# Kernel optimization log

Hardware: AMD Instinct MI355X
Metric: run time of the kernel (lower is better)

## Reference

```python
import jax, jax.numpy as jnp
import numpy as np


def setup_inputs() -> dict:
    key = jax.random.key(0)
    kq, kk, kv = jax.random.split(key, 3)
    B, S, D = 4, 4096, 128
    return {
        "q_proj": jax.random.normal(kq, (B, S, D), dtype=jnp.float32),
        "k_proj": jax.random.normal(kk, (B, S, D), dtype=jnp.float32),
        "v_proj": jax.random.normal(kv, (B, S, D), dtype=jnp.float32),
    }


def reference(q_proj, k_proj, v_proj):
    # Block-wise online softmax in the original is mathematically exact
    # full (non-causal) scaled dot-product attention.
    d = q_proj.shape[-1]
    scale = 1.0 / jnp.sqrt(jnp.asarray(d, dtype=q_proj.dtype))
    logits = jnp.einsum('bqd,bkd->bqk', q_proj, k_proj) * scale  # [B,S,S]
    attn = jax.nn.softmax(logits, axis=-1)
    return jnp.einsum('bqk,bkd->bqd', attn, v_proj)
```

## Files before the change

kernel.cpp:

```cpp
#include <hip/hip_runtime.h>
#include <hip/hip_bf16.h>
#include <stdint.h>

#define Bn 4
#define Sn 4096
#define Dn 128
#define SCALE ((float)(0.08838834764831843 * 1.4426950408889634))

typedef __attribute__((ext_vector_type(8)))  short short8;
typedef __attribute__((ext_vector_type(4)))  short short4v;
typedef __attribute__((ext_vector_type(4)))  float f32x4;
typedef __attribute__((ext_vector_type(16))) float f32x16;
typedef __attribute__((ext_vector_type(2)))  uint32_t uint2v;

__device__ __forceinline__ uint32_t bfround(float f){
  union { float f; uint32_t u; } a; a.f = f;
  return a.u + 0x7FFFu + ((a.u >> 16) & 1u);
}
__device__ __forceinline__ uint32_t f2bf2(float lo, float hi){
  return (bfround(hi) & 0xFFFF0000u) | (bfround(lo) >> 16);
}
__device__ __forceinline__ uint32_t f2bf2_fast(float lo, float hi){
  const uint32_t a = __float_as_uint(lo) + 0x8000u;
  const uint32_t b = __float_as_uint(hi) + 0x8000u;
  return __builtin_amdgcn_perm(b, a, 0x07060302u);
}
__device__ __forceinline__ float bf2f(short s){
  union { uint32_t u; float f; } a; a.u = ((uint32_t)(unsigned short)s) << 16; return a.f;
}
__device__ __forceinline__ float fexp2(float x){
#if __has_builtin(__builtin_amdgcn_exp2f)
  return __builtin_amdgcn_exp2f(x);
#else
  return exp2f(x);
#endif
}

__device__ __forceinline__ void gload16(const void* g, void* l){
  __builtin_amdgcn_global_load_lds(
      (const __attribute__((address_space(1))) unsigned int*)g,
      (__attribute__((address_space(3))) unsigned int*)l, 16, 0, 0);
}

__global__ void prep_kernel(const float* __restrict__ k, const float* __restrict__ v,
                            short* __restrict__ kb, short* __restrict__ vf){
  const int bid = blockIdx.x;
  const int t   = threadIdx.x;
  if (bid < 512){
    const int b = bid >> 7, i = bid & 127;
#pragma unroll
    for (int it=0; it<2; ++it){
      const int lin = it*256 + t;
      const int ln = lin & 31;
      const int tg = lin >> 5;
      const int tt = tg >> 1, hh = tg & 1;
      const float* src = k + ((size_t)(b*Sn + i*32 + ln))*Dn + tg*8;
      const f32x4 a = *(const f32x4*)src;
      const f32x4 c = *(const f32x4*)(src + 4);
      union { uint32_t u[4]; short8 s; } pk;
      pk.u[0] = f2bf2(a[0], a[1]);
      pk.u[1] = f2bf2(a[2], a[3]);
      pk.u[2] = f2bf2(c[0], c[1]);
      pk.u[3] = f2bf2(c[2], c[3]);
      *(short8*)(kb + (((size_t)(b*128 + i)*8 + tt)*64 + (hh*32 + ln))*8) = pk.s;
    }
  } else {
    __shared__ float tile[32][132];
    const int vb = bid - 512;
    const int b = vb >> 7, i = vb & 127;
#pragma unroll
    for (int it=0; it<4; ++it){
      const int lin = it*256 + t;
      const int row = lin >> 5;
      const int c4  = lin & 31;
      const f32x4 val = *(const f32x4*)(v + ((size_t)(b*Sn + i*32 + row))*Dn + c4*4);
      tile[row][c4*4+0] = val[0];
      tile[row][c4*4+1] = val[1];
      tile[row][c4*4+2] = val[2];
      tile[row][c4*4+3] = val[3];
    }
    __syncthreads();
#pragma unroll
    for (int cc=0; cc<2; ++cc){
      const int c = cc*256 + t;
      const int l = c & 63, fidx = c >> 6;
      const int t_ = fidx >> 2, mt = fidx & 3;
      const int ln = l & 31, h5 = l >> 5;
      const int d = mt*32 + ln;
      const int kb0 = 16*t_ + 4*h5;
      union { uint32_t u[4]; short8 s; } pk;
#pragma unroll
      for (int p=0;p<4;++p){
        const int j0 = 2*p, j1 = 2*p+1;
        const int kl0 = kb0 + (j0&3) + 8*(j0>>2);
        const int kl1 = kb0 + (j1&3) + 8*(j1>>2);
        pk.u[p] = f2bf2(tile[kl0][d], tile[kl1][d]);
      }
      *(short8*)(vf + (((size_t)(b*128 + i)*8 + fidx)*64 + l)*8) = pk.s;
    }
  }
}

__global__ __launch_bounds__(128, 2) void fa_kernel(
    const float* __restrict__ Qg, const short* __restrict__ Kb,
    const short* __restrict__ VFb, short* __restrict__ parts,
    float* __restrict__ lparts){
  __shared__ __align__(16) char lds[32768];
  const int tid = threadIdx.x;
  const int w = tid >> 6, lane = tid & 63;
  const int ln = lane & 31, h5 = lane >> 5;
  const int idx = blockIdx.x;
  const int b   = idx & 3;
  const int u2  = idx >> 2;
  const int qt  = u2 & 31;
  const int ks  = u2 >> 5;
  const int q0  = qt * 128;
  const int start_it = ks*21 + (ks < 2 ? ks : 2);
  const int n_it     = 21 + (ks < 2 ? 1 : 0);

  short8 Qf[2][8];
#pragma unroll
  for (int tile=0;tile<2;++tile){
    const float* qp = Qg + ((size_t)(b*Sn + q0 + w*64 + tile*32 + ln))*Dn;
#pragma unroll
    for (int t=0;t<8;++t){
      const int d0 = t*16 + h5*8;
      const f32x4 a = *(const f32x4*)(qp + d0);
      const f32x4 c = *(const f32x4*)(qp + d0 + 4);
      union { uint32_t u[4]; short8 s; } pk;
      pk.u[0] = f2bf2(a[0]*SCALE, a[1]*SCALE);
      pk.u[1] = f2bf2(a[2]*SCALE, a[3]*SCALE);
      pk.u[2] = f2bf2(c[0]*SCALE, c[1]*SCALE);
      pk.u[3] = f2bf2(c[2]*SCALE, c[3]*SCALE);
      Qf[tile][t] = pk.s;
    }
  }

  f32x16 Ot[2][4];
#pragma unroll
  for (int tile=0;tile<2;++tile)
#pragma unroll
    for (int m=0;m<4;++m)
#pragma unroll
      for (int r=0;r<16;++r) Ot[tile][m][r] = 0.0f;
  float ls00=0.f, ls01=0.f, ls10=0.f, ls11=0.f;

  const char* gsrc0 = (w ? (const char*)VFb : (const char*)Kb)
                    + (size_t)(b*128)*8192 + (size_t)lane*16;
  auto stage = [&](int it, int ph){
    char* dst = lds + ph*16384 + (w ? 8192 : 0);
    const char* src = gsrc0 + (size_t)it*8192;
#pragma unroll
    for (int u=0;u<8;++u) gload16(src + u*1024, dst + u*1024);
  };

  stage(start_it, 0);

  for (int i=0; i<n_it; ++i){
    const int ph = i & 1;
    __syncthreads();
    if (i+1 < n_it) stage(start_it+i+1, ph^1);

    const char* bK = lds + ph*16384 + (size_t)lane*16;
    const char* bV = bK + 8192;

    f32x16 St0, St1;
#pragma unroll
    for (int r=0;r<16;++r){ St0[r] = 0.0f; St1[r] = 0.0f; }
    __builtin_amdgcn_s_setprio(1);
#pragma unroll
    for (int t=0;t<8;++t){
      const short8 kf = *(const short8*)(bK + t*1024);
      St0 = __builtin_amdgcn_mfma_f32_32x32x16_bf16(kf, Qf[0][t], St0, 0, 0, 0);
      St1 = __builtin_amdgcn_mfma_f32_32x32x16_bf16(kf, Qf[1][t], St1, 0, 0, 0);
    }
    __builtin_amdgcn_s_setprio(0);

#pragma unroll
    for (int r=0;r<16;++r) St0[r] = fexp2(St0[r]);
#pragma unroll
    for (int r=0;r<16;++r) St1[r] = fexp2(St1[r]);
#pragma unroll
    for (int r=0;r<16;r+=2){
      ls00 += St0[r]; ls01 += St0[r+1];
      ls10 += St1[r]; ls11 += St1[r+1];
    }

    union { uint32_t u[4]; short8 s; } pfA[2], pfB[2];
#pragma unroll
    for (int t=0;t<2;++t){
      pfA[t].u[0] = f2bf2_fast(St0[8*t+0], St0[8*t+1]);
      pfA[t].u[1] = f2bf2_fast(St0[8*t+2], St0[8*t+3]);
      pfA[t].u[2] = f2bf2_fast(St0[8*t+4], St0[8*t+5]);
      pfA[t].u[3] = f2bf2_fast(St0[8*t+6], St0[8*t+7]);
      pfB[t].u[0] = f2bf2_fast(St1[8*t+0], St1[8*t+1]);
      pfB[t].u[1] = f2bf2_fast(St1[8*t+2], St1[8*t+3]);
      pfB[t].u[2] = f2bf2_fast(St1[8*t+4], St1[8*t+5]);
      pfB[t].u[3] = f2bf2_fast(St1[8*t+6], St1[8*t+7]);
    }

    __builtin_amdgcn_s_setprio(1);
#pragma unroll
    for (int t=0;t<2;++t){
#pragma unroll
      for (int mt=0;mt<4;++mt){
        const short8 vf = *(const short8*)(bV + (t*4+mt)*1024);
        Ot[0][mt] = __builtin_amdgcn_mfma_f32_32x32x16_bf16(vf, pfA[t].s, Ot[0][mt], 0, 0, 0);
        Ot[1][mt] = __builtin_amdgcn_mfma_f32_32x32x16_bf16(vf, pfB[t].s, Ot[1][mt], 0, 0, 0);
      }
    }
    __builtin_amdgcn_s_setprio(0);
  }

  float lsum0 = ls00 + ls01; lsum0 += __shfl_xor(lsum0, 32, 64);
  float lsum1 = ls10 + ls11; lsum1 += __shfl_xor(lsum1, 32, 64);

  const int pslot = (b*32 + qt)*6 + ks;
#pragma unroll
  for (int tile=0;tile<2;++tile){
    short* pbase = parts + (size_t)pslot*16384 + (size_t)(w*64 + tile*32 + ln)*128;
#pragma unroll
    for (int mt=0;mt<4;++mt){
#pragma unroll
      for (int g=0;g<4;++g){
        union { uint32_t u[2]; short4v s; } o;
        o.u[0] = f2bf2(Ot[tile][mt][4*g],   Ot[tile][mt][4*g+1]);
        o.u[1] = f2bf2(Ot[tile][mt][4*g+2], Ot[tile][mt][4*g+3]);
        *(short4v*)(pbase + mt*32 + 8*g + 4*h5) = o.s;
      }
    }
  }
  if (h5 == 0){
    lparts[(size_t)pslot*128 + w*64 + ln]      = lsum0;
    lparts[(size_t)pslot*128 + w*64 + 32 + ln] = lsum1;
  }
}

__global__ void reduce_kernel(const short* __restrict__ parts,
                              const float* __restrict__ lparts,
                              float* __restrict__ out){
  const int t  = threadIdx.x;
  const int s  = blockIdx.x >> 3;
  const int qg = (blockIdx.x & 7)*16 + (t >> 4);
  const int d0 = (t & 15) * 8;
  float acc[8];
#pragma unroll
  for (int j=0;j<8;++j) acc[j] = 0.0f;
  float lsum = 0.0f;
#pragma unroll
  for (int ks=0;ks<6;++ks){
    const short8 p = *(const short8*)(parts + ((size_t)(s*6+ks))*16384 + (size_t)qg*128 + d0);
#pragma unroll
    for (int j=0;j<8;++j) acc[j] += bf2f(p[j]);
    lsum += lparts[(size_t)(s*6+ks)*128 + qg];
  }
  const float linv = 1.0f / lsum;
  f32x4 o0, o1;
#pragma unroll
  for (int j=0;j<4;++j){ o0[j] = acc[j]*linv; o1[j] = acc[4+j]*linv; }
  float* op = out + ((size_t)(s*128 + qg))*128 + d0;
  *(f32x4*)op = o0;
  *(f32x4*)(op + 4) = o1;
}

extern "C" void kernel_launch(void* const* d_in, const int* in_sizes, int n_in,
                              void* d_out, int out_size, void* d_ws, size_t ws_size,
                              hipStream_t stream){
  const float* q = (const float*)d_in[0];
  const float* k = (const float*)d_in[1];
  const float* v = (const float*)d_in[2];
  float* out = (float*)d_out;
  char* ws = (char*)d_ws;
  short* kb     = (short*)ws;
  short* vfb    = kb + (size_t)Bn*Sn*Dn;
  short* parts  = (short*)(ws + 8388608);
  float* lparts = (float*)(ws + 8388608 + 25165824);

  prep_kernel<<<1024, 256, 0, stream>>>(k, v, kb, vfb);
  fa_kernel<<<768, 128, 0, stream>>>(q, kb, vfb, parts, lparts);
  reduce_kernel<<<1024, 256, 0, stream>>>(parts, lparts, out);
}
```

Baseline: 123.5 us.

## Fuse split-K reduction into attention kernel via last-block atomic counter

Removes the separate reduce kernel launch. Each query tile's eight key-split blocks now bump an atomic counter, and the last block to finish sums the bf16 partials and writes the normalized output. The key range is split into 8 equal chunks of 16 iterations instead of 6 uneven ones, giving 1024 blocks. This saves one launch and its tail, at the cost of a serialized reduction done by one 128-thread block per tile, plus fence and atomic overhead.

```diff
diff --git a/kernel.cpp b/kernel.cpp
--- a/kernel.cpp
+++ b/kernel.cpp
@@ -43,9 +43,11 @@
 }
 
 __global__ void prep_kernel(const float* __restrict__ k, const float* __restrict__ v,
-                            short* __restrict__ kb, short* __restrict__ vf){
+                            short* __restrict__ kb, short* __restrict__ vf,
+                            int* __restrict__ cnt){
   const int bid = blockIdx.x;
   const int t   = threadIdx.x;
+  if (bid == 0 && t < 128) cnt[t] = 0;
   if (bid < 512){
     const int b = bid >> 7, i = bid & 127;
 #pragma unroll
@@ -104,8 +106,10 @@
 __global__ __launch_bounds__(128, 2) void fa_kernel(
     const float* __restrict__ Qg, const short* __restrict__ Kb,
     const short* __restrict__ VFb, short* __restrict__ parts,
-    float* __restrict__ lparts){
+    float* __restrict__ lparts, int* __restrict__ cnt,
+    float* __restrict__ out){
   __shared__ __align__(16) char lds[32768];
+  __shared__ int isLast;
   const int tid = threadIdx.x;
   const int w = tid >> 6, lane = tid & 63;
   const int ln = lane & 31, h5 = lane >> 5;
@@ -115,8 +119,8 @@
   const int qt  = u2 & 31;
   const int ks  = u2 >> 5;
   const int q0  = qt * 128;
-  const int start_it = ks*21 + (ks < 2 ? ks : 2);
-  const int n_it     = 21 + (ks < 2 ? 1 : 0);
+  const int start_it = ks * 16;
+  const int n_it     = 16;
 
   short8 Qf[2][8];
 #pragma unroll
@@ -215,7 +219,8 @@
   float lsum0 = ls00 + ls01; lsum0 += __shfl_xor(lsum0, 32, 64);
   float lsum1 = ls10 + ls11; lsum1 += __shfl_xor(lsum1, 32, 64);
 
-  const int pslot = (b*32 + qt)*6 + ks;
+  const int slot  = b*32 + qt;
+  const int pslot = slot*8 + ks;
 #pragma unroll
   for (int tile=0;tile<2;++tile){
     short* pbase = parts + (size_t)pslot*16384 + (size_t)(w*64 + tile*32 + ln)*128;
@@ -234,33 +239,42 @@
     lparts[(size_t)pslot*128 + w*64 + ln]      = lsum0;
     lparts[(size_t)pslot*128 + w*64 + 32 + ln] = lsum1;
   }
-}
-
-__global__ void reduce_kernel(const short* __restrict__ parts,
-                              const float* __restrict__ lparts,
-                              float* __restrict__ out){
-  const int t  = threadIdx.x;
-  const int s  = blockIdx.x >> 3;
-  const int qg = (blockIdx.x & 7)*16 + (t >> 4);
-  const int d0 = (t & 15) * 8;
-  float acc[8];
-#pragma unroll
-  for (int j=0;j<8;++j) acc[j] = 0.0f;
-  float lsum = 0.0f;
-#pragma unroll
-  for (int ks=0;ks<6;++ks){
-    const short8 p = *(const short8*)(parts + ((size_t)(s*6+ks))*16384 + (size_t)qg*128 + d0);
-#pragma unroll
-    for (int j=0;j<8;++j) acc[j] += bf2f(p[j]);
-    lsum += lparts[(size_t)(s*6+ks)*128 + qg];
-  }
-  const float linv = 1.0f / lsum;
-  f32x4 o0, o1;
-#pragma unroll
-  for (int j=0;j<4;++j){ o0[j] = acc[j]*linv; o1[j] = acc[4+j]*linv; }
-  float* op = out + ((size_t)(s*128 + qg))*128 + d0;
-  *(f32x4*)op = o0;
-  *(f32x4*)(op + 4) = o1;
+
+  __threadfence();
+  __syncthreads();
+  if (tid == 0){
+    const int old = atomicAdd(cnt + slot, 1);
+    isLast = (old == 7);
+  }
+  __syncthreads();
+  if (!isLast) return;
+  __threadfence();
+
+  const short* pb = parts + (size_t)slot*8*16384;
+  const float* lb = lparts + (size_t)slot*8*128;
+#pragma unroll 1
+  for (int rr=0; rr<16; ++rr){
+    const int qg = rr*8 + (tid >> 4);
+    const int d0 = (tid & 15) * 8;
+    float acc[8];
+#pragma unroll
+    for (int j=0;j<8;++j) acc[j] = 0.0f;
+    float lsum = 0.0f;
+#pragma unroll
+    for (int k2=0;k2<8;++k2){
+      const short8 p = *(const short8*)(pb + (size_t)k2*16384 + (size_t)qg*128 + d0);
+#pragma unroll
+      for (int j=0;j<8;++j) acc[j] += bf2f(p[j]);
+      lsum += lb[k2*128 + qg];
+    }
+    const float linv = 1.0f / lsum;
+    f32x4 o0, o1;
+#pragma unroll
+    for (int j=0;j<4;++j){ o0[j] = acc[j]*linv; o1[j] = acc[4+j]*linv; }
+    float* op = out + ((size_t)(b*Sn + q0 + qg))*Dn + d0;
+    *(f32x4*)op = o0;
+    *(f32x4*)(op + 4) = o1;
+  }
 }
 
 extern "C" void kernel_launch(void* const* d_in, const int* in_sizes, int n_in,
@@ -274,9 +288,9 @@
   short* kb     = (short*)ws;
   short* vfb    = kb + (size_t)Bn*Sn*Dn;
   short* parts  = (short*)(ws + 8388608);
-  float* lparts = (float*)(ws + 8388608 + 25165824);
-
-  prep_kernel<<<1024, 256, 0, stream>>>(k, v, kb, vfb);
-  fa_kernel<<<768, 128, 0, stream>>>(q, kb, vfb, parts, lparts);
-  reduce_kernel<<<1024, 256, 0, stream>>>(parts, lparts, out);
-}
+  float* lparts = (float*)(ws + 8388608 + 33554432);
+  int*   cnt    = (int*)(ws + 8388608 + 33554432 + 524288);
+
+  prep_kernel<<<1024, 256, 0, stream>>>(k, v, kb, vfb, cnt);
+  fa_kernel<<<1024, 128, 0, stream>>>(q, kb, vfb, parts, lparts, cnt, out);
+}
```

Measured after the change: 220.4 us. 1.78x slower.
